# Kernel optimization log

Hardware: AMD Instinct MI355X
Metric: run time of the kernel (lower is better)

## Reference

```python
import jax, jax.numpy as jnp
import numpy as np
import math


def _build_coeffs(max_l):
    """Replicates RSHxyz._init_coefficients with exact integer/half-integer math.
    Returns (dst_pointers[T], clm_tuvs[T], xpows[T], ypows[T], zpows[T], ns_lms[(max_l+1)^2]).
    """
    dst, clm, px, py, pz, ns = [], [], [], [], [], []
    for l in range(max_l + 1):
        for m in range(-l, l + 1):
            am = abs(m)
            # ns_lm = 1/(2^|m| l!) * sqrt(2 (l+|m|)! (l-|m|)! / 2^(m==0))
            ns.append(
                1.0 / (2 ** am * math.factorial(l))
                * math.sqrt(2.0 * math.factorial(l + am) * math.factorial(l - am)
                            / (2.0 if m == 0 else 1.0))
            )
            # v is half-integer when m<0; track v2 = 2*v as an int
            v2_start = 1 if m < 0 else 0  # vm(m) = 0.5*(m<0), v starts at vm
            v2_stop = 2 * ((am - 1) // 2 if m < 0 else am // 2) + v2_start  # inclusive
            for t in range((l - am) // 2 + 1):
                for u in range(t + 1):
                    for v2 in range(v2_start, v2_stop + 1, 2):
                        parity = (t + (v2 - v2_start) // 2) % 2  # t + v - vm(m)
                        c = ((-1.0 if parity else 1.0)
                             * 0.25 ** t
                             * math.comb(l, t)
                             * (math.comb(l - t, am + t) if am + t <= l - t else 0)
                             * math.comb(t, u)
                             * (math.comb(am, v2) if v2 <= am else 0))
                        dst.append(l * (l + 1) + m)
                        clm.append(c)
                        px.append(2 * t + am - 2 * u - v2)
                        py.append(2 * u + v2)
                        pz.append(l - 2 * t - am)
    return (np.asarray(dst, np.int32), np.asarray(clm, np.float32),
            np.asarray(px, np.int32), np.asarray(py, np.int32),
            np.asarray(pz, np.int32), np.asarray(ns, np.float32))


def setup_inputs() -> dict:
    max_l = 6
    N = 500_000
    dst, clm, px, py, pz, ns = _build_coeffs(max_l)
    key = jax.random.key(0)
    xyz = jax.random.normal(key, (N, 3), dtype=jnp.float32)
    return {
        "xyz": xyz,
        "clm_tuvs": jnp.asarray(clm),
        "ns_lms": jnp.asarray(ns),
        "dst_pointers": jnp.asarray(dst),
        "xpows": jnp.asarray(px),
        "ypows": jnp.asarray(py),
        "zpows": jnp.asarray(pz),
        "max_l": max_l,
    }


def _pow_table(x, max_pow):
    # [N] -> [N, max_pow+1] with col k = x**k, built by repeated multiply so
    # negative bases and 0**0==1 are handled exactly (matches torch masked pow).
    cols = [jnp.ones_like(x)]
    for _ in range(max_pow):
        cols.append(cols[-1] * x)
    return jnp.stack(cols, axis=-1)


def reference(xyz, clm_tuvs, ns_lms, dst_pointers, xpows, ypows, zpows, max_l):
    xyz = xyz.reshape(-1, 3)
    tx = _pow_table(xyz[:, 0], max_l)  # [N, max_l+1]
    ty = _pow_table(xyz[:, 1], max_l)
    tz = _pow_table(xyz[:, 2], max_l)
    # monomials x^px * y^py * z^pz scaled by C^{lm}_{tuv}: [N, T]
    poly = tx[:, xpows] * ty[:, ypows] * tz[:, zpows] * clm_tuvs
    n_out = ns_lms.shape[0]  # (max_l+1)^2
    out = jnp.zeros((poly.shape[0], n_out), poly.dtype).at[:, dst_pointers].add(poly)
    return out * ns_lms
```

## Files before the change

### kernel.cpp

```cpp
#include <hip/hip_runtime.h>


namespace {

constexpr int MAXL   = 6;
constexpr int NOUT   = (MAXL + 1) * (MAXL + 1);
constexpr int NT_MAX = 256;

struct Tab {
    int   dst[NT_MAX];
    int   px[NT_MAX];
    int   py[NT_MAX];
    int   pz[NT_MAX];
    float clm[NT_MAX];
    int   cnt;
};

constexpr long long comb(int n, int k) {
    if (k < 0 || k > n) return 0;
    long long r = 1;
    for (int i = 0; i < k; ++i) r = r * (n - i) / (i + 1);
    return r;
}

constexpr Tab build_tab() {
    Tab tb{};
    int k = 0;
    for (int l = 0; l <= MAXL; ++l) {
        for (int m = -l; m <= l; ++m) {
            const int am  = (m < 0) ? -m : m;
            const int v2s = (m < 0) ? 1 : 0;
            const int v2e = 2 * ((m < 0) ? (am - 1) / 2 : am / 2) + v2s;
            for (int t = 0; t <= (l - am) / 2; ++t) {
                for (int u = 0; u <= t; ++u) {
                    for (int v2 = v2s; v2 <= v2e; v2 += 2) {
                        const int parity = (t + (v2 - v2s) / 2) % 2;
                        double c = parity ? -1.0 : 1.0;
                        for (int i = 0; i < t; ++i) c *= 0.25;
                        c *= (double)comb(l, t);
                        c *= (double)((am + t <= l - t) ? comb(l - t, am + t) : 0);
                        c *= (double)comb(t, u);
                        c *= (double)((v2 <= am) ? comb(am, v2) : 0);
                        tb.dst[k] = l * (l + 1) + m;
                        tb.px[k]  = 2 * t + am - 2 * u - v2;
                        tb.py[k]  = 2 * u + v2;
                        tb.pz[k]  = l - 2 * t - am;
                        tb.clm[k] = (float)c;
                        ++k;
                    }
                }
            }
        }
    }
    tb.cnt = k;
    return tb;
}

constexpr Tab TB = build_tab();
static_assert(TB.cnt == 188, "expected 188 terms for max_l=6");

constexpr int BLOCK = 256;

}

__global__ __launch_bounds__(BLOCK) void rsh_kernel(const float* __restrict__ xyz,
                                                    const float* __restrict__ ns,
                                                    float* __restrict__ out,
                                                    int N) {
    __shared__ float sm[BLOCK * NOUT];

    const int tid = threadIdx.x;
    const long long i = (long long)blockIdx.x * BLOCK + tid;

    float x = 0.f, y = 0.f, z = 0.f;
    if (i < N) {
        const float* p = xyz + i * 3;
        x = p[0]; y = p[1]; z = p[2];
    }

    float xp[MAXL + 1], yp[MAXL + 1], zp[MAXL + 1];
    xp[0] = yp[0] = zp[0] = 1.f;
#pragma unroll
    for (int p = 1; p <= MAXL; ++p) {
        xp[p] = xp[p - 1] * x;
        yp[p] = yp[p - 1] * y;
        zp[p] = zp[p - 1] * z;
    }

    float acc[NOUT];
#pragma unroll
    for (int o = 0; o < NOUT; ++o) acc[o] = 0.f;

#pragma unroll
    for (int k = 0; k < TB.cnt; ++k) {
        const float mono = xp[TB.px[k]] * yp[TB.py[k]] * zp[TB.pz[k]];
        acc[TB.dst[k]] = fmaf(TB.clm[k], mono, acc[TB.dst[k]]);
    }

#pragma unroll
    for (int o = 0; o < NOUT; ++o) sm[tid * NOUT + o] = acc[o] * ns[o];

    __syncthreads();

    const float4* sm4 = (const float4*)sm;
    float4* out4 = (float4*)out;
    const long long base4 = (long long)blockIdx.x * (BLOCK * NOUT / 4);
    const long long lim4 = (long long)N * NOUT / 4;
#pragma unroll 1
    for (int idx = tid; idx < BLOCK * NOUT / 4; idx += BLOCK) {
        const long long g = base4 + idx;
        if (g < lim4) out4[g] = sm4[idx];
    }
}

extern "C" void kernel_launch(void* const* d_in, const int* in_sizes, int n_in,
                              void* d_out, int out_size, void* d_ws, size_t ws_size,
                              hipStream_t stream) {
    const float* xyz = (const float*)d_in[0];
    const float* ns  = (const float*)d_in[2];
    float* out = (float*)d_out;

    const int N = in_sizes[0] / 3;
    const int grid = (N + BLOCK - 1) / BLOCK;
    rsh_kernel<<<grid, BLOCK, 0, stream>>>(xyz, ns, out, N);
}
```

Before: 118.4 us.

## Fold normalization into coefficients, stream accumulators to LDS, use nontemporal stores

```diff
diff --git a/kernel.cpp b/kernel.cpp
--- a/kernel.cpp
+++ b/kernel.cpp
@@ -7,12 +7,15 @@
 constexpr int NOUT   = (MAXL + 1) * (MAXL + 1);
 constexpr int NT_MAX = 256;
 
+typedef float f4 __attribute__((ext_vector_type(4)));
+
 struct Tab {
-    int   dst[NT_MAX];
     int   px[NT_MAX];
     int   py[NT_MAX];
     int   pz[NT_MAX];
     float clm[NT_MAX];
+    int   dst[NT_MAX];
+    bool  last[NT_MAX];
     int   cnt;
 };
 
@@ -23,12 +26,28 @@
     return r;
 }
 
+constexpr double dfact(int n) {
+    double r = 1.0;
+    for (int i = 2; i <= n; ++i) r *= (double)i;
+    return r;
+}
+
+constexpr double csqrt(double x) {
+    double g = x > 1.0 ? x : 1.0;
+    for (int i = 0; i < 64; ++i) g = 0.5 * (g + x / g);
+    return g;
+}
+
 constexpr Tab build_tab() {
     Tab tb{};
     int k = 0;
     for (int l = 0; l <= MAXL; ++l) {
         for (int m = -l; m <= l; ++m) {
             const int am  = (m < 0) ? -m : m;
+            double ns = 1.0;
+            for (int i = 0; i < am; ++i) ns *= 0.5;
+            ns = ns / dfact(l)
+               * csqrt(2.0 * dfact(l + am) * dfact(l - am) / (m == 0 ? 2.0 : 1.0));
             const int v2s = (m < 0) ? 1 : 0;
             const int v2e = 2 * ((m < 0) ? (am - 1) / 2 : am / 2) + v2s;
             for (int t = 0; t <= (l - am) / 2; ++t) {
@@ -45,11 +64,13 @@
                         tb.px[k]  = 2 * t + am - 2 * u - v2;
                         tb.py[k]  = 2 * u + v2;
                         tb.pz[k]  = l - 2 * t - am;
-                        tb.clm[k] = (float)c;
+                        tb.clm[k] = (float)(c * ns);
+                        tb.last[k] = false;
                         ++k;
                     }
                 }
             }
+            tb.last[k - 1] = true;
         }
     }
     tb.cnt = k;
@@ -59,22 +80,23 @@
 constexpr Tab TB = build_tab();
 static_assert(TB.cnt == 188, "expected 188 terms for max_l=6");
 
-constexpr int BLOCK = 256;
+constexpr int BLOCK = 128;
+constexpr int SLAB4 = BLOCK * NOUT / 4;
 
 }
 
 __global__ __launch_bounds__(BLOCK) void rsh_kernel(const float* __restrict__ xyz,
-                                                    const float* __restrict__ ns,
                                                     float* __restrict__ out,
                                                     int N) {
     __shared__ float sm[BLOCK * NOUT];
 
     const int tid = threadIdx.x;
-    const long long i = (long long)blockIdx.x * BLOCK + tid;
+    const int blk = blockIdx.x;
+    const int i   = blk * BLOCK + tid;
 
     float x = 0.f, y = 0.f, z = 0.f;
     if (i < N) {
-        const float* p = xyz + i * 3;
+        const float* p = xyz + (long long)i * 3;
         x = p[0]; y = p[1]; z = p[2];
     }
 
@@ -87,29 +109,36 @@
         zp[p] = zp[p - 1] * z;
     }
 
-    float acc[NOUT];
-#pragma unroll
-    for (int o = 0; o < NOUT; ++o) acc[o] = 0.f;
-
+    float acc = 0.f;
 #pragma unroll
     for (int k = 0; k < TB.cnt; ++k) {
-        const float mono = xp[TB.px[k]] * yp[TB.py[k]] * zp[TB.pz[k]];
-        acc[TB.dst[k]] = fmaf(TB.clm[k], mono, acc[TB.dst[k]]);
+        acc = fmaf(TB.clm[k], xp[TB.px[k]] * yp[TB.py[k]] * zp[TB.pz[k]], acc);
+        if (TB.last[k]) {
+            sm[tid * NOUT + TB.dst[k]] = acc;
+            acc = 0.f;
+        }
     }
-
-#pragma unroll
-    for (int o = 0; o < NOUT; ++o) sm[tid * NOUT + o] = acc[o] * ns[o];
 
     __syncthreads();
 
-    const float4* sm4 = (const float4*)sm;
-    float4* out4 = (float4*)out;
-    const long long base4 = (long long)blockIdx.x * (BLOCK * NOUT / 4);
-    const long long lim4 = (long long)N * NOUT / 4;
-#pragma unroll 1
-    for (int idx = tid; idx < BLOCK * NOUT / 4; idx += BLOCK) {
-        const long long g = base4 + idx;
-        if (g < lim4) out4[g] = sm4[idx];
+    const f4* s4 = (const f4*)sm;
+    f4* o4 = (f4*)out;
+    const int base4 = blk * SLAB4;
+    const int lim4  = (N * NOUT) >> 2;
+    const int remF  = (N * NOUT) & 3;
+#pragma unroll
+    for (int it = 0; it < SLAB4 / BLOCK + 1; ++it) {
+        const int f = it * BLOCK + tid;
+        if (f < SLAB4) {
+            const int g = base4 + f;
+            if (g < lim4) {
+                __builtin_nontemporal_store(s4[f], o4 + g);
+            } else if (g == lim4 && remF) {
+#pragma unroll
+                for (int t = 0; t < 3; ++t)
+                    if (t < remF) out[(long long)g * 4 + t] = sm[f * 4 + t];
+            }
+        }
     }
 }
 
@@ -117,10 +146,9 @@
                               void* d_out, int out_size, void* d_ws, size_t ws_size,
                               hipStream_t stream) {
     const float* xyz = (const float*)d_in[0];
-    const float* ns  = (const float*)d_in[2];
     float* out = (float*)d_out;
 
     const int N = in_sizes[0] / 3;
     const int grid = (N + BLOCK - 1) / BLOCK;
-    rsh_kernel<<<grid, BLOCK, 0, stream>>>(xyz, ns, out, N);
+    rsh_kernel<<<grid, BLOCK, 0, stream>>>(xyz, out, N);
 }
```

Result: slower. 123.6 us (+4.4%).
